# Optimization experiments

Hardware: AMD Instinct MI355X
Metric: run time of the kernel (lower is better)

## Reference

```python
import jax, jax.numpy as jnp
import numpy as np

N = 100000   # entities
T = 4        # edge types
E = 250000   # edges per type
D = 64       # dimension
H = 4        # attention heads
C = 64       # per-head out channels (PyG out_channels)
F_IN = 256   # raw feature dim
L = 2        # num_layers
NEG_SLOPE = 0.2


def setup_inputs() -> dict:
    key = jax.random.key(0)
    ks = jax.random.split(key, 10)
    return {
        "feature_matrix": jax.random.normal(ks[0], (N, F_IN), jnp.float32),
        "entity_emb": jax.random.normal(ks[1], (N + 1, D), jnp.float32),
        "lin_w": jax.random.normal(ks[2], (F_IN, D), jnp.float32) * 0.05,
        "lin_b": jnp.zeros((D,), jnp.float32),
        "ln_g": jnp.ones((D,), jnp.float32),
        "ln_b": jnp.zeros((D,), jnp.float32),
        "W_src": jax.random.normal(ks[3], (L, T, D, H * C), jnp.float32) * 0.1,
        "W_dst": jax.random.normal(ks[4], (L, T, D, H * C), jnp.float32) * 0.1,
        "a_src": jax.random.normal(ks[5], (L, T, H, C), jnp.float32) * 0.1,
        "a_dst": jax.random.normal(ks[6], (L, T, H, C), jnp.float32) * 0.1,
        "conv_bias": jnp.zeros((L, T, C), jnp.float32),
        "edge_index": jax.random.randint(ks[7], (T, 2, E), 0, N, jnp.int32),
    }


def _layer_norm(x, g, b):
    mu = jnp.mean(x, axis=-1, keepdims=True)
    var = jnp.var(x, axis=-1, keepdims=True)
    return (x - mu) * jax.lax.rsqrt(var + 1e-5) * g + b


def _l2_normalize(x):
    n = jnp.linalg.norm(x, axis=-1, keepdims=True)
    return x / jnp.maximum(n, 1e-12)


def _gat_conv(x, src, dst, Ws, Wd, a_s, a_d, bias):
    # x: [N, D]; src/dst: [E'] (self loops already appended, PyG default)
    xs = (x @ Ws).reshape(N, H, C)          # source projection per head
    xd = (x @ Wd).reshape(N, H, C)          # destination projection per head
    logit = (xs * a_s).sum(-1)[src] + (xd * a_d).sum(-1)[dst]  # [E', H]
    logit = jax.nn.leaky_relu(logit, NEG_SLOPE)
    # segment softmax over incoming edges of each dst node
    m = jax.lax.stop_gradient(jax.ops.segment_max(logit, dst, num_segments=N))
    p = jnp.exp(logit - m[dst])
    s = jax.ops.segment_sum(p, dst, num_segments=N)
    alpha = p / s[dst]                       # [E', H]
    msg = xs[src] * alpha[..., None]         # [E', H, C]
    out = jax.ops.segment_sum(msg.reshape(-1, H * C), dst, num_segments=N)
    out = out.reshape(N, H, C).mean(axis=1)  # concat=False -> head mean
    return out + bias


def reference(feature_matrix, entity_emb, lin_w, lin_b, ln_g, ln_b,
              W_src, W_dst, a_src, a_dst, conv_bias, edge_index):
    # feature_transform: Linear -> LayerNorm -> GELU (exact erf GELU, torch default)
    xf = jax.nn.gelu(_layer_norm(feature_matrix @ lin_w + lin_b, ln_g, ln_b),
                     approximate=False)
    xe = _l2_normalize(entity_emb[:N])
    x = xf + xe
    loop = jnp.arange(N, dtype=edge_index.dtype)
    for l in range(L):
        acc = jnp.zeros((N, C), x.dtype)
        for t in range(T):
            src = jnp.concatenate([edge_index[t, 0], loop])
            dst = jnp.concatenate([edge_index[t, 1], loop])
            acc = acc + _gat_conv(x, src, dst, W_src[l, t], W_dst[l, t],
                                  a_src[l, t], a_dst[l, t], conv_bias[l, t])
        x = jax.nn.gelu(acc / T, approximate=False)  # HeteroConv aggr='mean'; dropout=eval identity
    return x
```

## Files before the change

### kernel.cpp

```cpp
#include <hip/hip_runtime.h>
#include <hip/hip_bf16.h>
#include <cstdint>

#define NN   100000
#define TT   4
#define EE   250000
#define LL   2
#define NCH  49
#define N64  ((size_t)NN * 64)

typedef unsigned short ushort_t;
typedef __attribute__((ext_vector_type(8))) short bf16x8;
typedef __attribute__((ext_vector_type(16))) float floatx16;
typedef __attribute__((ext_vector_type(4))) float floatx4;

static __device__ __forceinline__ float gelu_exact(float v) {
    return 0.5f * v * (1.0f + erff(v * 0.7071067811865476f));
}
static __device__ __forceinline__ float wave_sum64(float v) {
    #pragma unroll
    for (int m = 32; m; m >>= 1) v += __shfl_xor(v, m, 64);
    return v;
}
static __device__ __forceinline__ ushort_t f2bf(float f) {
    unsigned u = __float_as_uint(f);
    u += 0x7FFFu + ((u >> 16) & 1u);
    return (ushort_t)(u >> 16);
}
static __device__ __forceinline__ float bf2f(ushort_t h) {
    return __uint_as_float((unsigned)h << 16);
}
static __device__ __forceinline__ void gl_lds16(const ushort_t* g, ushort_t* l) {
    __builtin_amdgcn_global_load_lds(
        (const __attribute__((address_space(1))) void*)g,
        (__attribute__((address_space(3))) void*)l, 16, 0, 0);
}

__global__ __launch_bounds__(256) void k_prep(
    const float* __restrict__ Wsrc, const float* __restrict__ Wdst,
    const float* __restrict__ asrc, const float* __restrict__ adst,
    const float* __restrict__ cb, const float* __restrict__ lin_w,
    ushort_t* __restrict__ wcTh, ushort_t* __restrict__ wcTl,
    ushort_t* __restrict__ lwTh, ushort_t* __restrict__ lwTl,
    ushort_t* __restrict__ bpTh, ushort_t* __restrict__ bpTl,
    float* __restrict__ bsum)
{
    int id = blockIdx.x * 256 + threadIdx.x;
    {
        int d = id & 63;
        int c = (id >> 6) & 63;
        int h = (id >> 12) & 3;
        int t = (id >> 14) & 3;
        int l = (id >> 16) & 1;
        float v = 0.25f * Wsrc[(((l * 4 + t) * 64 + d) * 256) + h * 64 + c];
        int dst = (l * 64 + c) * 1024 + (t * 256 + h * 64 + d);
        ushort_t hh = f2bf(v);
        bpTh[dst] = hh;
        bpTl[dst] = f2bf(v - bf2f(hh));
    }
    if (id < LL * 64 * 64) {
        int d   = id & 63;
        int col = (id >> 6) & 63;
        int l   = (id >> 12) & 1;
        int t = col >> 3, side = (col >> 2) & 1, h = col & 3;
        const float* W = side ? Wdst : Wsrc;
        const float* a = side ? adst : asrc;
        int wb = ((l * 4 + t) * 64 + d) * 256 + h * 64;
        int ab = ((l * 4 + t) * 4 + h) * 64;
        float s = 0.f;
        #pragma unroll 8
        for (int c2 = 0; c2 < 64; ++c2) s = fmaf(W[wb + c2], a[ab + c2], s);
        int dst = (l * 64 + col) * 64 + d;
        ushort_t hh = f2bf(s);
        wcTh[dst] = hh;
        wcTl[dst] = f2bf(s - bf2f(hh));
    }
    if (id < 64 * 256) {
        int k = id & 255, c = id >> 8;
        float v = lin_w[k * 64 + c];
        ushort_t hh = f2bf(v);
        lwTh[c * 256 + k] = hh;
        lwTl[c * 256 + k] = f2bf(v - bf2f(hh));
    }
    if (id < LL * 64) {
        int l = id >> 6, c = id & 63;
        float s = 0.f;
        for (int t = 0; t < TT; ++t) s += cb[(l * 4 + t) * 64 + c];
        bsum[id] = s;
    }
}

__global__ void k_hist(const int* __restrict__ ei, int* __restrict__ cursor) {
    int id = blockIdx.x * 256 + threadIdx.x;
    if (id >= TT * EE) return;
    int t = id / EE, e = id - t * EE;
    int d = ei[(t * 2 + 1) * EE + e];
    atomicAdd(&cursor[t * NN + d], 1);
}

__global__ __launch_bounds__(256) void k_scan1(const int* __restrict__ deg,
                                               int* __restrict__ csum) {
    int b = blockIdx.x, t = b / NCH, cc = b - t * NCH;
    int tid = threadIdx.x;
    int base = cc * 2048 + tid * 8;
    int s = 0;
    #pragma unroll
    for (int i = 0; i < 8; ++i) {
        int idx = base + i;
        if (idx < NN) s += deg[t * NN + idx];
    }
    #pragma unroll
    for (int m = 32; m; m >>= 1) s += __shfl_xor(s, m, 64);
    __shared__ int ws4[4];
    int lane = tid & 63, wid = tid >> 6;
    if (lane == 0) ws4[wid] = s;
    __syncthreads();
    if (tid == 0) csum[b] = ws4[0] + ws4[1] + ws4[2] + ws4[3];
}

__global__ void k_scan2(const int* __restrict__ csum, int* __restrict__ cbase,
                        int* __restrict__ row_ptr) {
    int t = threadIdx.x;
    if (t >= TT) return;
    int base = 0;
    for (int c = 0; c < NCH; ++c) {
        cbase[t * NCH + c] = base;
        base += csum[t * NCH + c];
    }
    row_ptr[t * (NN + 1) + NN] = base;
}

__global__ __launch_bounds__(256) void k_scan3(int* __restrict__ cursor,
                                               const int* __restrict__ cbase,
                                               int* __restrict__ row_ptr) {
    int b = blockIdx.x, t = b / NCH, cc = b - t * NCH;
    int tid = threadIdx.x, lane = tid & 63, wid = tid >> 6;
    int base = cc * 2048 + tid * 8;
    int vals[8], ts = 0;
    #pragma unroll
    for (int i = 0; i < 8; ++i) {
        int idx = base + i;
        int v = (idx < NN) ? cursor[t * NN + idx] : 0;
        vals[i] = v; ts += v;
    }
    int v = ts;
    #pragma unroll
    for (int off = 1; off < 64; off <<= 1) {
        int u = __shfl_up(v, off, 64);
        if (lane >= off) v += u;
    }
    __shared__ int wt[4];
    if (lane == 63) wt[wid] = v;
    __syncthreads();
    int wbase = 0;
    for (int w = 0; w < wid; ++w) wbase += wt[w];
    int run = cbase[t * NCH + cc] + wbase + (v - ts);
    #pragma unroll
    for (int i = 0; i < 8; ++i) {
        int idx = base + i;
        if (idx < NN) {
            row_ptr[t * (NN + 1) + idx] = run;
            cursor[t * NN + idx] = run;
        }
        run += vals[i];
    }
}

__global__ void k_scatter(const int* __restrict__ ei, int* __restrict__ cursor,
                          int2* __restrict__ sd) {
    int id = blockIdx.x * 256 + threadIdx.x;
    if (id >= TT * EE) return;
    int t = id / EE, r = id - t * EE;
    int s = ei[t * 2 * EE + r];
    int d = ei[(t * 2 + 1) * EE + r];
    int pos = atomicAdd(&cursor[t * NN + d], 1);
    sd[(size_t)t * EE + pos] = make_int2(s, d);
}

__global__ __launch_bounds__(256, 4) void k_gemm_f32a(
    const float* __restrict__ Af,
    const ushort_t* __restrict__ Bhi, const ushort_t* __restrict__ Blo,
    int K, int ldb, int nrows, float* __restrict__ Cout)
{
    constexpr int KC = 32;
    __shared__ ushort_t sAh[128 * 32], sAl[128 * 32];
    __shared__ ushort_t sBh[64 * 32],  sBl[64 * 32];
    const int tid = threadIdx.x;
    const int w = tid >> 6, ln = tid & 63;
    const int l31 = ln & 31, hl = ln >> 5;
    const int rowbase = blockIdx.x * 128;

    floatx16 accv[2];
    #pragma unroll
    for (int ct = 0; ct < 2; ++ct)
        #pragma unroll
        for (int r = 0; r < 16; ++r) accv[ct][r] = 0.f;

    for (int kc = 0; kc < K; kc += KC) {
        __syncthreads();
        #pragma unroll
        for (int i = 0; i < 2; ++i) {
            int f = tid + i * 256;
            int r = f >> 2, cg = f & 3;
            int row = rowbase + r;
            int sg = (r ^ (r >> 2)) & 3;
            int sw = r * 32 + ((cg ^ sg) << 3);
            if (row < nrows) {
                size_t ga = (size_t)row * K + kc + cg * 8;
                floatx4 v0 = *(const floatx4*)(Af + ga);
                floatx4 v1 = *(const floatx4*)(Af + ga + 4);
                float vf[8] = {v0.x, v0.y, v0.z, v0.w, v1.x, v1.y, v1.z, v1.w};
                unsigned hu[8], lu[8];
                #pragma unroll
                for (int q = 0; q < 8; ++q) {
                    ushort_t hh = f2bf(vf[q]);
                    hu[q] = hh;
                    lu[q] = f2bf(vf[q] - bf2f(hh));
                }
                uint4 H = make_uint4(hu[0] | (hu[1] << 16), hu[2] | (hu[3] << 16),
                                     hu[4] | (hu[5] << 16), hu[6] | (hu[7] << 16));
                uint4 L = make_uint4(lu[0] | (lu[1] << 16), lu[2] | (lu[3] << 16),
                                     lu[4] | (lu[5] << 16), lu[6] | (lu[7] << 16));
                *(uint4*)&sAh[sw] = H;
                *(uint4*)&sAl[sw] = L;
            } else {
                *(uint4*)&sAh[sw] = make_uint4(0, 0, 0, 0);
                *(uint4*)&sAl[sw] = make_uint4(0, 0, 0, 0);
            }
        }
        {
            int r = tid >> 2, cg = tid & 3;
            int sg = (r ^ (r >> 2)) & 3;
            int so = r * 32 + (cg << 3);
            size_t gb = (size_t)r * ldb + kc + ((cg ^ sg) << 3);
            gl_lds16(Bhi + gb, &sBh[so]);
            gl_lds16(Blo + gb, &sBl[so]);
        }
        __syncthreads();
        const int arow = (w << 5) + l31;
        const int sga = (arow ^ (arow >> 2)) & 3;
        const int sgb = (l31 ^ (l31 >> 2)) & 3;
        #pragma unroll
        for (int s = 0; s < 2; ++s) {
            const int c0 = (s << 1) | hl;
            const int ka = (c0 ^ sga) << 3;
            const int kb = (c0 ^ sgb) << 3;
            bf16x8 ah  = *(const bf16x8*)&sAh[arow * 32 + ka];
            bf16x8 al  = *(const bf16x8*)&sAl[arow * 32 + ka];
            bf16x8 bh0 = *(const bf16x8*)&sBh[l31 * 32 + kb];
            bf16x8 bl0 = *(const bf16x8*)&sBl[l31 * 32 + kb];
            bf16x8 bh1 = *(const bf16x8*)&sBh[(32 + l31) * 32 + kb];
            bf16x8 bl1 = *(const bf16x8*)&sBl[(32 + l31) * 32 + kb];
            accv[0] = __builtin_amdgcn_mfma_f32_32x32x16_bf16(ah, bh0, accv[0], 0, 0, 0);
            accv[1] = __builtin_amdgcn_mfma_f32_32x32x16_bf16(ah, bh1, accv[1], 0, 0, 0);
            accv[0] = __builtin_amdgcn_mfma_f32_32x32x16_bf16(al, bh0, accv[0], 0, 0, 0);
            accv[1] = __builtin_amdgcn_mfma_f32_32x32x16_bf16(al, bh1, accv[1], 0, 0, 0);
            accv[0] = __builtin_amdgcn_mfma_f32_32x32x16_bf16(ah, bl0, accv[0], 0, 0, 0);
            accv[1] = __builtin_amdgcn_mfma_f32_32x32x16_bf16(ah, bl1, accv[1], 0, 0, 0);
        }
    }
    #pragma unroll
    for (int ct = 0; ct < 2; ++ct) {
        int col = (ct << 5) + l31;
        #pragma unroll
        for (int r = 0; r < 16; ++r) {
            int row = rowbase + (w << 5) + (r & 3) + ((r >> 2) << 3) + (hl << 2);
            if (row < nrows) Cout[(size_t)row * 64 + col] = accv[ct][r];
        }
    }
}

template <int FLAGS>
__global__ __launch_bounds__(256, 6) void k_gemm64(
    const ushort_t* __restrict__ Ahi, const ushort_t* __restrict__ Alo,
    const ushort_t* __restrict__ Bhi, const ushort_t* __restrict__ Blo,
    int K, int ldb, int nrows,
    const float* __restrict__ accbuf, const float* __restrict__ bias,
    float* __restrict__ Cout)
{
    constexpr int KC = 32;
    __shared__ ushort_t sAh[64 * 32], sAl[64 * 32];
    __shared__ ushort_t sBh[64 * 32], sBl[64 * 32];
    const int tid = threadIdx.x;
    const int w = tid >> 6, ln = tid & 63;
    const int l31 = ln & 31, hl = ln >> 5;
    const int rt = w >> 1, ct = w & 1;
    const int rowbase = blockIdx.x * 64;

    floatx16 acc;
    #pragma unroll
    for (int r = 0; r < 16; ++r) acc[r] = 0.f;

    for (int kc = 0; kc < K; kc += KC) {
        __syncthreads();
        {
            int r = tid >> 2, cg = tid & 3;
            int sg = (r ^ (r >> 2)) & 3;
            int so = r * 32 + (cg << 3);
            int row = rowbase + r;
            if (row < nrows) {
                size_t ga = (size_t)row * K + kc + ((cg ^ sg) << 3);
                gl_lds16(Ahi + ga, &sAh[so]);
                gl_lds16(Alo + ga, &sAl[so]);
            }
            size_t gb = (size_t)r * ldb + kc + ((cg ^ sg) << 3);
            gl_lds16(Bhi + gb, &sBh[so]);
            gl_lds16(Blo + gb, &sBl[so]);
        }
        __syncthreads();
        const int arow = (rt << 5) + l31;
        const int brow = (ct << 5) + l31;
        const int sga = (arow ^ (arow >> 2)) & 3;
        const int sgb = (l31 ^ (l31 >> 2)) & 3;
        #pragma unroll
        for (int s = 0; s < 2; ++s) {
            const int c0 = (s << 1) | hl;
            const int ka = (c0 ^ sga) << 3;
            const int kb = (c0 ^ sgb) << 3;
            bf16x8 ah = *(const bf16x8*)&sAh[arow * 32 + ka];
            bf16x8 al = *(const bf16x8*)&sAl[arow * 32 + ka];
            bf16x8 bh = *(const bf16x8*)&sBh[brow * 32 + kb];
            bf16x8 bl = *(const bf16x8*)&sBl[brow * 32 + kb];
            acc = __builtin_amdgcn_mfma_f32_32x32x16_bf16(ah, bh, acc, 0, 0, 0);
            acc = __builtin_amdgcn_mfma_f32_32x32x16_bf16(al, bh, acc, 0, 0, 0);
            acc = __builtin_amdgcn_mfma_f32_32x32x16_bf16(ah, bl, acc, 0, 0, 0);
        }
    }
    int col = (ct << 5) + l31;
    float bv = (FLAGS & 2) ? bias[col] : 0.f;
    #pragma unroll
    for (int r = 0; r < 16; ++r) {
        int row = rowbase + (rt << 5) + (r & 3) + ((r >> 2) << 3) + (hl << 2);
        if (row < nrows) {
            size_t idx = (size_t)row * 64 + col;
            float v = acc[r];
            if (FLAGS & 1) v += accbuf[idx];
            if (FLAGS & 2) v = gelu_exact((v + bv) * 0.25f);
            Cout[idx] = v;
        }
    }
}

__global__ __launch_bounds__(256) void k_feat_post(
    const float* __restrict__ y, const float* __restrict__ lin_b,
    const float* __restrict__ ln_g, const float* __restrict__ ln_b,
    const float* __restrict__ emb, float* __restrict__ xout)
{
    int n = (blockIdx.x << 2) + (threadIdx.x >> 6);
    int c = threadIdx.x & 63;
    size_t base = (size_t)n * 64 + c;
    float v = y[base] + lin_b[c];
    float mean = wave_sum64(v) * 0.015625f;
    float t = v - mean;
    float var = wave_sum64(t * t) * 0.015625f;
    float vn = t * (1.0f / sqrtf(var + 1e-5f)) * ln_g[c] + ln_b[c];
    float g = gelu_exact(vn);
    float e = emb[base];
    float nrm = sqrtf(wave_sum64(e * e));
    float xv = g + e / fmaxf(nrm, 1e-12f);
    xout[base] = xv;
}

__global__ __launch_bounds__(256) void k_edgep(
    const float* __restrict__ s_all, const int2* __restrict__ sd,
    float* __restrict__ parr)
{
    int i = blockIdx.x * 256 + threadIdx.x;
    int t = blockIdx.y;
    if (i >= EE) return;
    size_t base = (size_t)t * EE + i;
    int2 e = sd[base];
    const float4 a = *(const float4*)&s_all[(size_t)e.x * 64 + t * 8];
    const float4 b = *(const float4*)&s_all[(size_t)e.y * 64 + t * 8 + 4];
    float l0 = a.x + b.x, l1 = a.y + b.y;
    float l2 = a.z + b.z, l3 = a.w + b.w;
    l0 = l0 > 0.f ? l0 : 0.2f * l0;
    l1 = l1 > 0.f ? l1 : 0.2f * l1;
    l2 = l2 > 0.f ? l2 : 0.2f * l2;
    l3 = l3 > 0.f ? l3 : 0.2f * l3;
    float4 p = make_float4(__expf(l0), __expf(l1), __expf(l2), __expf(l3));
    *(float4*)&parr[base * 4] = p;
}

__global__ __launch_bounds__(256) void k_edge2(
    const float* __restrict__ x, const float* __restrict__ s_all,
    const float* __restrict__ parr, const int* __restrict__ row_ptr,
    const int2* __restrict__ sd,
    ushort_t* __restrict__ zh, ushort_t* __restrict__ zl, int t0)
{
    int n = (blockIdx.x << 2) + (threadIdx.x >> 6);
    int lane = threadIdx.x & 63;
    const int tA = t0, tB = t0 + 1;
    int eA  = row_ptr[tA * (NN + 1) + n];
    int eA1 = row_ptr[tA * (NN + 1) + n + 1];
    int eB  = row_ptr[tB * (NN + 1) + n];
    int eB1 = row_ptr[tB * (NN + 1) + n + 1];
    const int*     sA = (const int*)(sd + (size_t)tA * EE);
    const floatx4* pA = (const floatx4*)parr + (size_t)tA * EE;
    const int*     sB = (const int*)(sd + (size_t)tB * EE);
    const floatx4* pB = (const floatx4*)parr + (size_t)tB * EE;
    float xn = x[(size_t)n * 64 + lane];
    float a0, a1, a2, a3, SA0, SA1, SA2, SA3;
    float b0, b1, b2, b3, SB0, SB1, SB2, SB3;
    {
        const float4 sa = *(const float4*)&s_all[(size_t)n * 64 + tA * 8];
        const float4 sb = *(const float4*)&s_all[(size_t)n * 64 + tA * 8 + 4];
        float l0 = sa.x + sb.x, l1 = sa.y + sb.y;
        float l2 = sa.z + sb.z, l3 = sa.w + sb.w;
        l0 = l0 > 0.f ? l0 : 0.2f * l0;  l1 = l1 > 0.f ? l1 : 0.2f * l1;
        l2 = l2 > 0.f ? l2 : 0.2f * l2;  l3 = l3 > 0.f ? l3 : 0.2f * l3;
        SA0 = __expf(l0); SA1 = __expf(l1); SA2 = __expf(l2); SA3 = __expf(l3);
        a0 = SA0 * xn; a1 = SA1 * xn; a2 = SA2 * xn; a3 = SA3 * xn;
    }
    {
        const float4 sa = *(const float4*)&s_all[(size_t)n * 64 + tB * 8];
        const float4 sb = *(const float4*)&s_all[(size_t)n * 64 + tB * 8 + 4];
        float l0 = sa.x + sb.x, l1 = sa.y + sb.y;
        float l2 = sa.z + sb.z, l3 = sa.w + sb.w;
        l0 = l0 > 0.f ? l0 : 0.2f * l0;  l1 = l1 > 0.f ? l1 : 0.2f * l1;
        l2 = l2 > 0.f ? l2 : 0.2f * l2;  l3 = l3 > 0.f ? l3 : 0.2f * l3;
        SB0 = __expf(l0); SB1 = __expf(l1); SB2 = __expf(l2); SB3 = __expf(l3);
        b0 = SB0 * xn; b1 = SB1 * xn; b2 = SB2 * xn; b3 = SB3 * xn;
    }
    int m = (eA1 - eA < eB1 - eB) ? (eA1 - eA) : (eB1 - eB);
    #pragma unroll 2
    for (int i = 0; i < m; ++i) {
        int sA_ = sA[2 * (eA + i)];
        int sB_ = sB[2 * (eB + i)];
        floatx4 pa = pA[eA + i];
        floatx4 pb = pB[eB + i];
        float xa = x[(size_t)sA_ * 64 + lane];
        float xb = x[(size_t)sB_ * 64 + lane];
        SA0 += pa.x; SA1 += pa.y; SA2 += pa.z; SA3 += pa.w;
        SB0 += pb.x; SB1 += pb.y; SB2 += pb.z; SB3 += pb.w;
        a0 = fmaf(pa.x, xa, a0); a1 = fmaf(pa.y, xa, a1);
        a2 = fmaf(pa.z, xa, a2); a3 = fmaf(pa.w, xa, a3);
        b0 = fmaf(pb.x, xb, b0); b1 = fmaf(pb.y, xb, b1);
        b2 = fmaf(pb.z, xb, b2); b3 = fmaf(pb.w, xb, b3);
    }
    eA += m; eB += m;
    for (; eA < eA1; ++eA) {
        int s = sA[2 * eA]; floatx4 p = pA[eA];
        float xv = x[(size_t)s * 64 + lane];
        SA0 += p.x; SA1 += p.y; SA2 += p.z; SA3 += p.w;
        a0 = fmaf(p.x, xv, a0); a1 = fmaf(p.y, xv, a1);
        a2 = fmaf(p.z, xv, a2); a3 = fmaf(p.w, xv, a3);
    }
    for (; eB < eB1; ++eB) {
        int s = sB[2 * eB]; floatx4 p = pB[eB];
        float xv = x[(size_t)s * 64 + lane];
        SB0 += p.x; SB1 += p.y; SB2 += p.z; SB3 += p.w;
        b0 = fmaf(p.x, xv, b0); b1 = fmaf(p.y, xv, b1);
        b2 = fmaf(p.z, xv, b2); b3 = fmaf(p.w, xv, b3);
    }
    size_t zb = (size_t)n * 512 + lane;
    {
        float v0 = a0 / SA0, v1 = a1 / SA1, v2 = a2 / SA2, v3 = a3 / SA3;
        ushort_t h0 = f2bf(v0), h1 = f2bf(v1), h2 = f2bf(v2), h3 = f2bf(v3);
        zh[zb]       = h0;  zl[zb]       = f2bf(v0 - bf2f(h0));
        zh[zb + 64]  = h1;  zl[zb + 64]  = f2bf(v1 - bf2f(h1));
        zh[zb + 128] = h2;  zl[zb + 128] = f2bf(v2 - bf2f(h2));
        zh[zb + 192] = h3;  zl[zb + 192] = f2bf(v3 - bf2f(h3));
    }
    {
        size_t zc = zb + 256;
        float v0 = b0 / SB0, v1 = b1 / SB1, v2 = b2 / SB2, v3 = b3 / SB3;
        ushort_t h0 = f2bf(v0), h1 = f2bf(v1), h2 = f2bf(v2), h3 = f2bf(v3);
        zh[zc]       = h0;  zl[zc]       = f2bf(v0 - bf2f(h0));
        zh[zc + 64]  = h1;  zl[zc + 64]  = f2bf(v1 - bf2f(h1));
        zh[zc + 128] = h2;  zl[zc + 128] = f2bf(v2 - bf2f(h2));
        zh[zc + 192] = h3;  zl[zc + 192] = f2bf(v3 - bf2f(h3));
    }
}

extern "C" void kernel_launch(void* const* d_in, const int* in_sizes, int n_in,
                              void* d_out, int out_size, void* d_ws, size_t ws_size,
                              hipStream_t stream) {
    const float* fm    = (const float*)d_in[0];
    const float* emb   = (const float*)d_in[1];
    const float* lin_w = (const float*)d_in[2];
    const float* lin_b = (const float*)d_in[3];
    const float* ln_g  = (const float*)d_in[4];
    const float* ln_b  = (const float*)d_in[5];
    const float* Wsrc  = (const float*)d_in[6];
    const float* Wdst  = (const float*)d_in[7];
    const float* asrc  = (const float*)d_in[8];
    const float* adst  = (const float*)d_in[9];
    const float* cbias = (const float*)d_in[10];
    const int*   ei    = (const int*)d_in[11];
    float* out = (float*)d_out;
    (void)in_sizes; (void)n_in; (void)out_size; (void)ws_size;

    char* w = (char*)d_ws;
    size_t off = 0;
    auto alloc = [&](size_t bytes) -> void* {
        void* p = w + off;
        off += (bytes + 255) & ~(size_t)255;
        return p;
    };
    ushort_t* wcTh = (ushort_t*)alloc((size_t)LL * 64 * 64 * 2);
    ushort_t* wcTl = (ushort_t*)alloc((size_t)LL * 64 * 64 * 2);
    ushort_t* lwTh = (ushort_t*)alloc((size_t)64 * 256 * 2);
    ushort_t* lwTl = (ushort_t*)alloc((size_t)64 * 256 * 2);
    ushort_t* bpTh = (ushort_t*)alloc((size_t)LL * 64 * 1024 * 2);
    ushort_t* bpTl = (ushort_t*)alloc((size_t)LL * 64 * 1024 * 2);
    float* bsum    = (float*)alloc((size_t)LL * 64 * 4);
    int*   row_ptr = (int*)  alloc((size_t)TT * (NN + 1) * 4);
    int*   cursor  = (int*)  alloc((size_t)TT * NN * 4);
    int2*  sdarr   = (int2*) alloc((size_t)TT * EE * 8);
    float* parr    = (float*)alloc((size_t)TT * EE * 4 * 4);
    int*   csum    = (int*)  alloc((size_t)TT * NCH * 4);
    int*   cbase   = (int*)  alloc((size_t)TT * NCH * 4);
    float* x       = (float*)alloc(N64 * 4);
    float* s_all   = (float*)alloc(N64 * 4);
    float* accB    = (float*)alloc(N64 * 4);
    size_t planeE = (size_t)NN * 512;
    ushort_t* zh = (ushort_t*)alloc(2 * planeE * 2);
    ushort_t* zl = zh + planeE;

    hipMemsetAsync(cursor, 0, (size_t)TT * NN * 4, stream);
    k_prep<<<512, 256, 0, stream>>>(Wsrc, Wdst, asrc, adst, cbias, lin_w,
                                    wcTh, wcTl, lwTh, lwTl, bpTh, bpTl, bsum);
    k_hist<<<(TT * EE + 255) / 256, 256, 0, stream>>>(ei, cursor);
    k_scan1<<<TT * NCH, 256, 0, stream>>>(cursor, csum);
    k_scan2<<<1, 64, 0, stream>>>(csum, cbase, row_ptr);
    k_scan3<<<TT * NCH, 256, 0, stream>>>(cursor, cbase, row_ptr);
    k_scatter<<<(TT * EE + 255) / 256, 256, 0, stream>>>(ei, cursor, sdarr);

    const int GB  = (NN + 127) / 128;
    const int GB2 = (NN + 63) / 64;
    k_gemm_f32a<<<GB, 256, 0, stream>>>(fm, lwTh, lwTl, 256, 256, NN, accB);
    k_feat_post<<<NN / 4, 256, 0, stream>>>(accB, lin_b, ln_g, ln_b, emb, x);

    const dim3 gp((EE + 255) / 256, TT);
    for (int l = 0; l < LL; ++l) {
        float* dest = (l == 0) ? x : out;
        k_gemm_f32a<<<GB, 256, 0, stream>>>(x, wcTh + l * 4096, wcTl + l * 4096,
                                            64, 64, NN, s_all);
        k_edgep<<<gp, 256, 0, stream>>>(s_all, sdarr, parr);
        const ushort_t* Bh = bpTh + (size_t)l * 65536;
        const ushort_t* Bl = bpTl + (size_t)l * 65536;
        k_edge2<<<NN / 4, 256, 0, stream>>>(x, s_all, parr, row_ptr, sdarr,
                                            zh, zl, 0);
        k_gemm64<0><<<GB2, 256, 0, stream>>>(zh, zl, Bh, Bl, 512, 1024, NN,
                                             nullptr, nullptr, accB);
        k_edge2<<<NN / 4, 256, 0, stream>>>(x, s_all, parr, row_ptr, sdarr,
                                            zh, zl, 2);
        k_gemm64<3><<<GB2, 256, 0, stream>>>(zh, zl, Bh + 512, Bl + 512, 512, 1024,
                                             NN, accB, bsum + l * 64, dest);
    }
}
```

Baseline: 1.019 ms.

## Store edge aggregates as fp32 and split to bf16 hi/lo inside GEMM

The edge aggregation kernel now writes fp32 results instead of two bf16 hi/lo planes. The GEMM loads fp32 A tiles and does the hi/lo split itself before writing to LDS, replacing the async global-to-LDS copies. Each edge wave now handles two nodes (n and n+N/2) so more independent gather loads are in flight. The intermediate traffic stays the same size (fp32 equals hi+lo bf16), but the GEMM adds conversion ALU work and loses the direct LDS loads, while the edge kernel uses more registers.

```diff
diff --git a/kernel.cpp b/kernel.cpp
--- a/kernel.cpp
+++ b/kernel.cpp
@@ -271,8 +271,8 @@
 }
 
 template <int FLAGS>
-__global__ __launch_bounds__(256, 6) void k_gemm64(
-    const ushort_t* __restrict__ Ahi, const ushort_t* __restrict__ Alo,
+__global__ __launch_bounds__(256, 6) void k_gemm64f(
+    const float* __restrict__ Af,
     const ushort_t* __restrict__ Bhi, const ushort_t* __restrict__ Blo,
     int K, int ldb, int nrows,
     const float* __restrict__ accbuf, const float* __restrict__ bias,
@@ -296,13 +296,31 @@
         {
             int r = tid >> 2, cg = tid & 3;
             int sg = (r ^ (r >> 2)) & 3;
+            int row = rowbase + r;
+            int sw = r * 32 + ((cg ^ sg) << 3);
+            if (row < nrows) {
+                size_t ga = (size_t)row * K + kc + cg * 8;
+                floatx4 v0 = *(const floatx4*)(Af + ga);
+                floatx4 v1 = *(const floatx4*)(Af + ga + 4);
+                float vf[8] = {v0.x, v0.y, v0.z, v0.w, v1.x, v1.y, v1.z, v1.w};
+                unsigned hu[8], lu[8];
+                #pragma unroll
+                for (int q = 0; q < 8; ++q) {
+                    ushort_t hh = f2bf(vf[q]);
+                    hu[q] = hh;
+                    lu[q] = f2bf(vf[q] - bf2f(hh));
+                }
+                uint4 H = make_uint4(hu[0] | (hu[1] << 16), hu[2] | (hu[3] << 16),
+                                     hu[4] | (hu[5] << 16), hu[6] | (hu[7] << 16));
+                uint4 L = make_uint4(lu[0] | (lu[1] << 16), lu[2] | (lu[3] << 16),
+                                     lu[4] | (lu[5] << 16), lu[6] | (lu[7] << 16));
+                *(uint4*)&sAh[sw] = H;
+                *(uint4*)&sAl[sw] = L;
+            } else {
+                *(uint4*)&sAh[sw] = make_uint4(0, 0, 0, 0);
+                *(uint4*)&sAl[sw] = make_uint4(0, 0, 0, 0);
+            }
             int so = r * 32 + (cg << 3);
-            int row = rowbase + r;
-            if (row < nrows) {
-                size_t ga = (size_t)row * K + kc + ((cg ^ sg) << 3);
-                gl_lds16(Ahi + ga, &sAh[so]);
-                gl_lds16(Alo + ga, &sAl[so]);
-            }
             size_t gb = (size_t)r * ldb + kc + ((cg ^ sg) << 3);
             gl_lds16(Bhi + gb, &sBh[so]);
             gl_lds16(Blo + gb, &sBl[so]);
@@ -382,94 +400,181 @@
     *(float4*)&parr[base * 4] = p;
 }
 
-__global__ __launch_bounds__(256) void k_edge2(
+__global__ __launch_bounds__(256, 6) void k_edge2(
     const float* __restrict__ x, const float* __restrict__ s_all,
     const float* __restrict__ parr, const int* __restrict__ row_ptr,
-    const int2* __restrict__ sd,
-    ushort_t* __restrict__ zh, ushort_t* __restrict__ zl, int t0)
+    const int2* __restrict__ sd, float* __restrict__ zf, int t0)
 {
-    int n = (blockIdx.x << 2) + (threadIdx.x >> 6);
+    int id = (blockIdx.x << 2) + (threadIdx.x >> 6);
     int lane = threadIdx.x & 63;
+    const int nA = id, nC = id + (NN / 2);
     const int tA = t0, tB = t0 + 1;
-    int eA  = row_ptr[tA * (NN + 1) + n];
-    int eA1 = row_ptr[tA * (NN + 1) + n + 1];
-    int eB  = row_ptr[tB * (NN + 1) + n];
-    int eB1 = row_ptr[tB * (NN + 1) + n + 1];
-    const int*     sA = (const int*)(sd + (size_t)tA * EE);
-    const floatx4* pA = (const floatx4*)parr + (size_t)tA * EE;
-    const int*     sB = (const int*)(sd + (size_t)tB * EE);
-    const floatx4* pB = (const floatx4*)parr + (size_t)tB * EE;
-    float xn = x[(size_t)n * 64 + lane];
+    int eA = row_ptr[tA * (NN + 1) + nA], eA1 = row_ptr[tA * (NN + 1) + nA + 1];
+    int eB = row_ptr[tB * (NN + 1) + nA], eB1 = row_ptr[tB * (NN + 1) + nA + 1];
+    int eC = row_ptr[tA * (NN + 1) + nC], eC1 = row_ptr[tA * (NN + 1) + nC + 1];
+    int eD = row_ptr[tB * (NN + 1) + nC], eD1 = row_ptr[tB * (NN + 1) + nC + 1];
+    const int*     sAp = (const int*)(sd + (size_t)tA * EE);
+    const floatx4* pAp = (const floatx4*)parr + (size_t)tA * EE;
+    const int*     sBp = (const int*)(sd + (size_t)tB * EE);
+    const floatx4* pBp = (const floatx4*)parr + (size_t)tB * EE;
+
+    float xnA = x[(size_t)nA * 64 + lane];
+    float xnC = x[(size_t)nC * 64 + lane];
+
     float a0, a1, a2, a3, SA0, SA1, SA2, SA3;
     float b0, b1, b2, b3, SB0, SB1, SB2, SB3;
-    {
-        const float4 sa = *(const float4*)&s_all[(size_t)n * 64 + tA * 8];
-        const float4 sb = *(const float4*)&s_all[(size_t)n * 64 + tA * 8 + 4];
+    float c0, c1, c2, c3, SC0, SC1, SC2, SC3;
+    float d0, d1, d2, d3, SD0, SD1, SD2, SD3;
+    {
+        const float4 sa = *(const float4*)&s_all[(size_t)nA * 64 + tA * 8];
+        const float4 sb = *(const float4*)&s_all[(size_t)nA * 64 + tA * 8 + 4];
         float l0 = sa.x + sb.x, l1 = sa.y + sb.y;
         float l2 = sa.z + sb.z, l3 = sa.w + sb.w;
         l0 = l0 > 0.f ? l0 : 0.2f * l0;  l1 = l1 > 0.f ? l1 : 0.2f * l1;
         l2 = l2 > 0.f ? l2 : 0.2f * l2;  l3 = l3 > 0.f ? l3 : 0.2f * l3;
         SA0 = __expf(l0); SA1 = __expf(l1); SA2 = __expf(l2); SA3 = __expf(l3);
-        a0 = SA0 * xn; a1 = SA1 * xn; a2 = SA2 * xn; a3 = SA3 * xn;
-    }
-    {
-        const float4 sa = *(const float4*)&s_all[(size_t)n * 64 + tB * 8];
-        const float4 sb = *(const float4*)&s_all[(size_t)n * 64 + tB * 8 + 4];
+        a0 = SA0 * xnA; a1 = SA1 * xnA; a2 = SA2 * xnA; a3 = SA3 * xnA;
+    }
+    {
+        const float4 sa = *(const float4*)&s_all[(size_t)nA * 64 + tB * 8];
+        const float4 sb = *(const float4*)&s_all[(size_t)nA * 64 + tB * 8 + 4];
         float l0 = sa.x + sb.x, l1 = sa.y + sb.y;
         float l2 = sa.z + sb.z, l3 = sa.w + sb.w;
         l0 = l0 > 0.f ? l0 : 0.2f * l0;  l1 = l1 > 0.f ? l1 : 0.2f * l1;
         l2 = l2 > 0.f ? l2 : 0.2f * l2;  l3 = l3 > 0.f ? l3 : 0.2f * l3;
         SB0 = __expf(l0); SB1 = __expf(l1); SB2 = __expf(l2); SB3 = __expf(l3);
-        b0 = SB0 * xn; b1 = SB1 * xn; b2 = SB2 * xn; b3 = SB3 * xn;
-    }
-    int m = (eA1 - eA < eB1 - eB) ? (eA1 - eA) : (eB1 - eB);
-    #pragma unroll 2
-    for (int i = 0; i < m; ++i) {
-        int sA_ = sA[2 * (eA + i)];
-        int sB_ = sB[2 * (eB + i)];
-        floatx4 pa = pA[eA + i];
-        floatx4 pb = pB[eB + i];
-        float xa = x[(size_t)sA_ * 64 + lane];
-        float xb = x[(size_t)sB_ * 64 + lane];
+        b0 = SB0 * xnA; b1 = SB1 * xnA; b2 = SB2 * xnA; b3 = SB3 * xnA;
+    }
+    {
+        const float4 sa = *(const float4*)&s_all[(size_t)nC * 64 + tA * 8];
+        const float4 sb = *(const float4*)&s_all[(size_t)nC * 64 + tA * 8 + 4];
+        float l0 = sa.x + sb.x, l1 = sa.y + sb.y;
+        float l2 = sa.z + sb.z, l3 = sa.w + sb.w;
+        l0 = l0 > 0.f ? l0 : 0.2f * l0;  l1 = l1 > 0.f ? l1 : 0.2f * l1;
+        l2 = l2 > 0.f ? l2 : 0.2f * l2;  l3 = l3 > 0.f ? l3 : 0.2f * l3;
+        SC0 = __expf(l0); SC1 = __expf(l1); SC2 = __expf(l2); SC3 = __expf(l3);
+        c0 = SC0 * xnC; c1 = SC1 * xnC; c2 = SC2 * xnC; c3 = SC3 * xnC;
+    }
+    {
+        const float4 sa = *(const float4*)&s_all[(size_t)nC * 64 + tB * 8];
+        const float4 sb = *(const float4*)&s_all[(size_t)nC * 64 + tB * 8 + 4];
+        float l0 = sa.x + sb.x, l1 = sa.y + sb.y;
+        float l2 = sa.z + sb.z, l3 = sa.w + sb.w;
+        l0 = l0 > 0.f ? l0 : 0.2f * l0;  l1 = l1 > 0.f ? l1 : 0.2f * l1;
+        l2 = l2 > 0.f ? l2 : 0.2f * l2;  l3 = l3 > 0.f ? l3 : 0.2f * l3;
+        SD0 = __expf(l0); SD1 = __expf(l1); SD2 = __expf(l2); SD3 = __expf(l3);
+        d0 = SD0 * xnC; d1 = SD1 * xnC; d2 = SD2 * xnC; d3 = SD3 * xnC;
+    }
+    int m4a = (eA1 - eA < eB1 - eB) ? (eA1 - eA) : (eB1 - eB);
+    int m4b = (eC1 - eC < eD1 - eD) ? (eC1 - eC) : (eD1 - eD);
+    int m4 = (m4a < m4b) ? m4a : m4b;
+    #pragma unroll 1
+    for (int q = 0; q < m4; ++q) {
+        int sA = sAp[2 * (eA + q)];
+        int sB = sBp[2 * (eB + q)];
+        int sC = sAp[2 * (eC + q)];
+        int sD = sBp[2 * (eD + q)];
+        floatx4 pa = pAp[eA + q];
+        floatx4 pb = pBp[eB + q];
+        floatx4 pc = pAp[eC + q];
+        floatx4 pd = pBp[eD + q];
+        float xa = x[(size_t)sA * 64 + lane];
+        float xb = x[(size_t)sB * 64 + lane];
+        float xc = x[(size_t)sC * 64 + lane];
+        float xd = x[(size_t)sD * 64 + lane];
         SA0 += pa.x; SA1 += pa.y; SA2 += pa.z; SA3 += pa.w;
         SB0 += pb.x; SB1 += pb.y; SB2 += pb.z; SB3 += pb.w;
+        SC0 += pc.x; SC1 += pc.y; SC2 += pc.z; SC3 += pc.w;
+        SD0 += pd.x; SD1 += pd.y; SD2 += pd.z; SD3 += pd.w;
         a0 = fmaf(pa.x, xa, a0); a1 = fmaf(pa.y, xa, a1);
         a2 = fmaf(pa.z, xa, a2); a3 = fmaf(pa.w, xa, a3);
         b0 = fmaf(pb.x, xb, b0); b1 = fmaf(pb.y, xb, b1);
         b2 = fmaf(pb.z, xb, b2); b3 = fmaf(pb.w, xb, b3);
-    }
-    eA += m; eB += m;
+        c0 = fmaf(pc.x, xc, c0); c1 = fmaf(pc.y, xc, c1);
+        c2 = fmaf(pc.z, xc, c2); c3 = fmaf(pc.w, xc, c3);
+        d0 = fmaf(pd.x, xd, d0); d1 = fmaf(pd.y, xd, d1);
+        d2 = fmaf(pd.z, xd, d2); d3 = fmaf(pd.w, xd, d3);
+    }
+    eA += m4; eB += m4; eC += m4; eD += m4;
+    {
+        int m2 = (eA1 - eA < eB1 - eB) ? (eA1 - eA) : (eB1 - eB);
+        #pragma unroll 2
+        for (int q = 0; q < m2; ++q) {
+            int sA = sAp[2 * (eA + q)];
+            int sB = sBp[2 * (eB + q)];
+            floatx4 pa = pAp[eA + q];
+            floatx4 pb = pBp[eB + q];
+            float xa = x[(size_t)sA * 64 + lane];
+            float xb = x[(size_t)sB * 64 + lane];
+            SA0 += pa.x; SA1 += pa.y; SA2 += pa.z; SA3 += pa.w;
+            SB0 += pb.x; SB1 += pb.y; SB2 += pb.z; SB3 += pb.w;
+            a0 = fmaf(pa.x, xa, a0); a1 = fmaf(pa.y, xa, a1);
+            a2 = fmaf(pa.z, xa, a2); a3 = fmaf(pa.w, xa, a3);
+            b0 = fmaf(pb.x, xb, b0); b1 = fmaf(pb.y, xb, b1);
+            b2 = fmaf(pb.z, xb, b2); b3 = fmaf(pb.w, xb, b3);
+        }
+        eA += m2; eB += m2;
+    }
+    {
+        int m2 = (eC1 - eC < eD1 - eD) ? (eC1 - eC) : (eD1 - eD);
+        #pragma unroll 2
+        for (int q = 0; q < m2; ++q) {
+            int sC = sAp[2 * (eC + q)];
+            int sD = sBp[2 * (eD + q)];
+            floatx4 pc = pAp[eC + q];
+            floatx4 pd = pBp[eD + q];
+            float xc = x[(size_t)sC * 64 + lane];
+            float xd = x[(size_t)sD * 64 + lane];
+            SC0 += pc.x; SC1 += pc.y; SC2 += pc.z; SC3 += pc.w;
+            SD0 += pd.x; SD1 += pd.y; SD2 += pd.z; SD3 += pd.w;
+            c0 = fmaf(pc.x, xc, c0); c1 = fmaf(pc.y, xc, c1);
+            c2 = fmaf(pc.z, xc, c2); c3 = fmaf(pc.w, xc, c3);
+            d0 = fmaf(pd.x, xd, d0); d1 = fmaf(pd.y, xd, d1);
+            d2 = fmaf(pd.z, xd, d2); d3 = fmaf(pd.w, xd, d3);
+        }
+        eC += m2; eD += m2;
+    }
     for (; eA < eA1; ++eA) {
-        int s = sA[2 * eA]; floatx4 p = pA[eA];
+        int s = sAp[2 * eA]; floatx4 p = pAp[eA];
         float xv = x[(size_t)s * 64 + lane];
         SA0 += p.x; SA1 += p.y; SA2 += p.z; SA3 += p.w;
         a0 = fmaf(p.x, xv, a0); a1 = fmaf(p.y, xv, a1);
         a2 = fmaf(p.z, xv, a2); a3 = fmaf(p.w, xv, a3);
     }
     for (; eB < eB1; ++eB) {
-        int s = sB[2 * eB]; floatx4 p = pB[eB];
+        int s = sBp[2 * eB]; floatx4 p = pBp[eB];
         float xv = x[(size_t)s * 64 + lane];
         SB0 += p.x; SB1 += p.y; SB2 += p.z; SB3 += p.w;
         b0 = fmaf(p.x, xv, b0); b1 = fmaf(p.y, xv, b1);
         b2 = fmaf(p.z, xv, b2); b3 = fmaf(p.w, xv, b3);
     }
-    size_t zb = (size_t)n * 512 + lane;
-    {
-        float v0 = a0 / SA0, v1 = a1 / SA1, v2 = a2 / SA2, v3 = a3 / SA3;
-        ushort_t h0 = f2bf(v0), h1 = f2bf(v1), h2 = f2bf(v2), h3 = f2bf(v3);
-        zh[zb]       = h0;  zl[zb]       = f2bf(v0 - bf2f(h0));
-        zh[zb + 64]  = h1;  zl[zb + 64]  = f2bf(v1 - bf2f(h1));
-        zh[zb + 128] = h2;  zl[zb + 128] = f2bf(v2 - bf2f(h2));
-        zh[zb + 192] = h3;  zl[zb + 192] = f2bf(v3 - bf2f(h3));
-    }
-    {
-        size_t zc = zb + 256;
-        float v0 = b0 / SB0, v1 = b1 / SB1, v2 = b2 / SB2, v3 = b3 / SB3;
-        ushort_t h0 = f2bf(v0), h1 = f2bf(v1), h2 = f2bf(v2), h3 = f2bf(v3);
-        zh[zc]       = h0;  zl[zc]       = f2bf(v0 - bf2f(h0));
-        zh[zc + 64]  = h1;  zl[zc + 64]  = f2bf(v1 - bf2f(h1));
-        zh[zc + 128] = h2;  zl[zc + 128] = f2bf(v2 - bf2f(h2));
-        zh[zc + 192] = h3;  zl[zc + 192] = f2bf(v3 - bf2f(h3));
+    for (; eC < eC1; ++eC) {
+        int s = sAp[2 * eC]; floatx4 p = pAp[eC];
+        float xv = x[(size_t)s * 64 + lane];
+        SC0 += p.x; SC1 += p.y; SC2 += p.z; SC3 += p.w;
+        c0 = fmaf(p.x, xv, c0); c1 = fmaf(p.y, xv, c1);
+        c2 = fmaf(p.z, xv, c2); c3 = fmaf(p.w, xv, c3);
+    }
+    for (; eD < eD1; ++eD) {
+        int s = sBp[2 * eD]; floatx4 p = pBp[eD];
+        float xv = x[(size_t)s * 64 + lane];
+        SD0 += p.x; SD1 += p.y; SD2 += p.z; SD3 += p.w;
+        d0 = fmaf(p.x, xv, d0); d1 = fmaf(p.y, xv, d1);
+        d2 = fmaf(p.z, xv, d2); d3 = fmaf(p.w, xv, d3);
+    }
+    {
+        size_t zb = (size_t)nA * 512 + lane;
+        zf[zb]       = a0 / SA0;  zf[zb + 64]  = a1 / SA1;
+        zf[zb + 128] = a2 / SA2;  zf[zb + 192] = a3 / SA3;
+        zf[zb + 256] = b0 / SB0;  zf[zb + 320] = b1 / SB1;
+        zf[zb + 384] = b2 / SB2;  zf[zb + 448] = b3 / SB3;
+    }
+    {
+        size_t zb = (size_t)nC * 512 + lane;
+        zf[zb]       = c0 / SC0;  zf[zb + 64]  = c1 / SC1;
+        zf[zb + 128] = c2 / SC2;  zf[zb + 192] = c3 / SC3;
+        zf[zb + 256] = d0 / SD0;  zf[zb + 320] = d1 / SD1;
+        zf[zb + 384] = d2 / SD2;  zf[zb + 448] = d3 / SD3;
     }
 }
 
@@ -514,9 +619,7 @@
     float* x       = (float*)alloc(N64 * 4);
     float* s_all   = (float*)alloc(N64 * 4);
     float* accB    = (float*)alloc(N64 * 4);
-    size_t planeE = (size_t)NN * 512;
-    ushort_t* zh = (ushort_t*)alloc(2 * planeE * 2);
-    ushort_t* zl = zh + planeE;
+    float* zf = (float*)alloc((size_t)NN * 512 * 4);
 
     hipMemsetAsync(cursor, 0, (size_t)TT * NN * 4, stream);
     k_prep<<<512, 256, 0, stream>>>(Wsrc, Wdst, asrc, adst, cbias, lin_w,
@@ -540,13 +643,11 @@
         k_edgep<<<gp, 256, 0, stream>>>(s_all, sdarr, parr);
         const ushort_t* Bh = bpTh + (size_t)l * 65536;
         const ushort_t* Bl = bpTl + (size_t)l * 65536;
-        k_edge2<<<NN / 4, 256, 0, stream>>>(x, s_all, parr, row_ptr, sdarr,
-                                            zh, zl, 0);
-        k_gemm64<0><<<GB2, 256, 0, stream>>>(zh, zl, Bh, Bl, 512, 1024, NN,
-                                             nullptr, nullptr, accB);
-        k_edge2<<<NN / 4, 256, 0, stream>>>(x, s_all, parr, row_ptr, sdarr,
-                                            zh, zl, 2);
-        k_gemm64<3><<<GB2, 256, 0, stream>>>(zh, zl, Bh + 512, Bl + 512, 512, 1024,
-                                             NN, accB, bsum + l * 64, dest);
-    }
-}
+        k_edge2<<<NN / 8, 256, 0, stream>>>(x, s_all, parr, row_ptr, sdarr, zf, 0);
+        k_gemm64f<0><<<GB2, 256, 0, stream>>>(zf, Bh, Bl, 512, 1024, NN,
+                                              nullptr, nullptr, accB);
+        k_edge2<<<NN / 8, 256, 0, stream>>>(x, s_all, parr, row_ptr, sdarr, zf, 2);
+        k_gemm64f<3><<<GB2, 256, 0, stream>>>(zf, Bh + 512, Bl + 512, 512, 1024,
+                                              NN, accB, bsum + l * 64, dest);
+    }
+}
```

After: 1.021 ms. No clear change (+0.2%).

## Process one edge type per pass with fp32 intermediate split inside GEMM

Applied to the files above, without the earlier changes.

The edge aggregation now handles a single edge type per launch, with each wave covering two destination nodes half the graph apart. It writes fp32 aggregated features instead of precomputed bf16 hi/lo planes. The GEMM loads the fp32 A tile and does the hi/lo bf16 split while staging it into shared memory. The aim is to shrink the intermediate buffer and cut memory traffic, at the cost of twice as many launches and extra conversion work in the GEMM, plus accumulation through accB across four passes.

```diff
diff --git a/kernel.cpp b/kernel.cpp
--- a/kernel.cpp
+++ b/kernel.cpp
@@ -271,8 +271,8 @@
 }
 
 template <int FLAGS>
-__global__ __launch_bounds__(256, 6) void k_gemm64(
-    const ushort_t* __restrict__ Ahi, const ushort_t* __restrict__ Alo,
+__global__ __launch_bounds__(256, 6) void k_gemm64f(
+    const float* __restrict__ Af,
     const ushort_t* __restrict__ Bhi, const ushort_t* __restrict__ Blo,
     int K, int ldb, int nrows,
     const float* __restrict__ accbuf, const float* __restrict__ bias,
@@ -296,13 +296,31 @@
         {
             int r = tid >> 2, cg = tid & 3;
             int sg = (r ^ (r >> 2)) & 3;
+            int row = rowbase + r;
+            int sw = r * 32 + ((cg ^ sg) << 3);
+            if (row < nrows) {
+                size_t ga = (size_t)row * K + kc + cg * 8;
+                floatx4 v0 = *(const floatx4*)(Af + ga);
+                floatx4 v1 = *(const floatx4*)(Af + ga + 4);
+                float vf[8] = {v0.x, v0.y, v0.z, v0.w, v1.x, v1.y, v1.z, v1.w};
+                unsigned hu[8], lu[8];
+                #pragma unroll
+                for (int q = 0; q < 8; ++q) {
+                    ushort_t hh = f2bf(vf[q]);
+                    hu[q] = hh;
+                    lu[q] = f2bf(vf[q] - bf2f(hh));
+                }
+                uint4 H = make_uint4(hu[0] | (hu[1] << 16), hu[2] | (hu[3] << 16),
+                                     hu[4] | (hu[5] << 16), hu[6] | (hu[7] << 16));
+                uint4 L = make_uint4(lu[0] | (lu[1] << 16), lu[2] | (lu[3] << 16),
+                                     lu[4] | (lu[5] << 16), lu[6] | (lu[7] << 16));
+                *(uint4*)&sAh[sw] = H;
+                *(uint4*)&sAl[sw] = L;
+            } else {
+                *(uint4*)&sAh[sw] = make_uint4(0, 0, 0, 0);
+                *(uint4*)&sAl[sw] = make_uint4(0, 0, 0, 0);
+            }
             int so = r * 32 + (cg << 3);
-            int row = rowbase + r;
-            if (row < nrows) {
-                size_t ga = (size_t)row * K + kc + ((cg ^ sg) << 3);
-                gl_lds16(Ahi + ga, &sAh[so]);
-                gl_lds16(Alo + ga, &sAl[so]);
-            }
             size_t gb = (size_t)r * ldb + kc + ((cg ^ sg) << 3);
             gl_lds16(Bhi + gb, &sBh[so]);
             gl_lds16(Blo + gb, &sBl[so]);
@@ -385,91 +403,81 @@
 __global__ __launch_bounds__(256) void k_edge2(
     const float* __restrict__ x, const float* __restrict__ s_all,
     const float* __restrict__ parr, const int* __restrict__ row_ptr,
-    const int2* __restrict__ sd,
-    ushort_t* __restrict__ zh, ushort_t* __restrict__ zl, int t0)
+    const int2* __restrict__ sd, float* __restrict__ zf, int t)
 {
-    int n = (blockIdx.x << 2) + (threadIdx.x >> 6);
+    int id = (blockIdx.x << 2) + (threadIdx.x >> 6);
     int lane = threadIdx.x & 63;
-    const int tA = t0, tB = t0 + 1;
-    int eA  = row_ptr[tA * (NN + 1) + n];
-    int eA1 = row_ptr[tA * (NN + 1) + n + 1];
-    int eB  = row_ptr[tB * (NN + 1) + n];
-    int eB1 = row_ptr[tB * (NN + 1) + n + 1];
-    const int*     sA = (const int*)(sd + (size_t)tA * EE);
-    const floatx4* pA = (const floatx4*)parr + (size_t)tA * EE;
-    const int*     sB = (const int*)(sd + (size_t)tB * EE);
-    const floatx4* pB = (const floatx4*)parr + (size_t)tB * EE;
-    float xn = x[(size_t)n * 64 + lane];
+    const int nA = id, nC = id + (NN / 2);
+    int eA = row_ptr[t * (NN + 1) + nA], eA1 = row_ptr[t * (NN + 1) + nA + 1];
+    int eC = row_ptr[t * (NN + 1) + nC], eC1 = row_ptr[t * (NN + 1) + nC + 1];
+    const int*     sp = (const int*)(sd + (size_t)t * EE);
+    const floatx4* pp = (const floatx4*)parr + (size_t)t * EE;
+
+    float xnA = x[(size_t)nA * 64 + lane];
+    float xnC = x[(size_t)nC * 64 + lane];
+
     float a0, a1, a2, a3, SA0, SA1, SA2, SA3;
-    float b0, b1, b2, b3, SB0, SB1, SB2, SB3;
+    float c0, c1, c2, c3, SC0, SC1, SC2, SC3;
     {
-        const float4 sa = *(const float4*)&s_all[(size_t)n * 64 + tA * 8];
-        const float4 sb = *(const float4*)&s_all[(size_t)n * 64 + tA * 8 + 4];
+        const float4 sa = *(const float4*)&s_all[(size_t)nA * 64 + t * 8];
+        const float4 sb = *(const float4*)&s_all[(size_t)nA * 64 + t * 8 + 4];
         float l0 = sa.x + sb.x, l1 = sa.y + sb.y;
         float l2 = sa.z + sb.z, l3 = sa.w + sb.w;
         l0 = l0 > 0.f ? l0 : 0.2f * l0;  l1 = l1 > 0.f ? l1 : 0.2f * l1;
         l2 = l2 > 0.f ? l2 : 0.2f * l2;  l3 = l3 > 0.f ? l3 : 0.2f * l3;
         SA0 = __expf(l0); SA1 = __expf(l1); SA2 = __expf(l2); SA3 = __expf(l3);
-        a0 = SA0 * xn; a1 = SA1 * xn; a2 = SA2 * xn; a3 = SA3 * xn;
+        a0 = SA0 * xnA; a1 = SA1 * xnA; a2 = SA2 * xnA; a3 = SA3 * xnA;
     }
     {
-        const float4 sa = *(const float4*)&s_all[(size_t)n * 64 + tB * 8];
-        const float4 sb = *(const float4*)&s_all[(size_t)n * 64 + tB * 8 + 4];
+        const float4 sa = *(const float4*)&s_all[(size_t)nC * 64 + t * 8];
+        const float4 sb = *(const float4*)&s_all[(size_t)nC * 64 + t * 8 + 4];
         float l0 = sa.x + sb.x, l1 = sa.y + sb.y;
         float l2 = sa.z + sb.z, l3 = sa.w + sb.w;
         l0 = l0 > 0.f ? l0 : 0.2f * l0;  l1 = l1 > 0.f ? l1 : 0.2f * l1;
         l2 = l2 > 0.f ? l2 : 0.2f * l2;  l3 = l3 > 0.f ? l3 : 0.2f * l3;
-        SB0 = __expf(l0); SB1 = __expf(l1); SB2 = __expf(l2); SB3 = __expf(l3);
-        b0 = SB0 * xn; b1 = SB1 * xn; b2 = SB2 * xn; b3 = SB3 * xn;
-    }
-    int m = (eA1 - eA < eB1 - eB) ? (eA1 - eA) : (eB1 - eB);
+        SC0 = __expf(l0); SC1 = __expf(l1); SC2 = __expf(l2); SC3 = __expf(l3);
+        c0 = SC0 * xnC; c1 = SC1 * xnC; c2 = SC2 * xnC; c3 = SC3 * xnC;
+    }
+    int m = (eA1 - eA < eC1 - eC) ? (eA1 - eA) : (eC1 - eC);
     #pragma unroll 2
-    for (int i = 0; i < m; ++i) {
-        int sA_ = sA[2 * (eA + i)];
-        int sB_ = sB[2 * (eB + i)];
-        floatx4 pa = pA[eA + i];
-        floatx4 pb = pB[eB + i];
-        float xa = x[(size_t)sA_ * 64 + lane];
-        float xb = x[(size_t)sB_ * 64 + lane];
+    for (int q = 0; q < m; ++q) {
+        int sA = sp[2 * (eA + q)];
+        int sC = sp[2 * (eC + q)];
+        floatx4 pa = pp[eA + q];
+        floatx4 pc = pp[eC + q];
+        float xa = x[(size_t)sA * 64 + lane];
+        float xc = x[(size_t)sC * 64 + lane];
         SA0 += pa.x; SA1 += pa.y; SA2 += pa.z; SA3 += pa.w;
-        SB0 += pb.x; SB1 += pb.y; SB2 += pb.z; SB3 += pb.w;
+        SC0 += pc.x; SC1 += pc.y; SC2 += pc.z; SC3 += pc.w;
         a0 = fmaf(pa.x, xa, a0); a1 = fmaf(pa.y, xa, a1);
         a2 = fmaf(pa.z, xa, a2); a3 = fmaf(pa.w, xa, a3);
-        b0 = fmaf(pb.x, xb, b0); b1 = fmaf(pb.y, xb, b1);
-        b2 = fmaf(pb.z, xb, b2); b3 = fmaf(pb.w, xb, b3);
-    }
-    eA += m; eB += m;
+        c0 = fmaf(pc.x, xc, c0); c1 = fmaf(pc.y, xc, c1);
+        c2 = fmaf(pc.z, xc, c2); c3 = fmaf(pc.w, xc, c3);
+    }
+    eA += m; eC += m;
     for (; eA < eA1; ++eA) {
-        int s = sA[2 * eA]; floatx4 p = pA[eA];
+        int s = sp[2 * eA]; floatx4 p = pp[eA];
         float xv = x[(size_t)s * 64 + lane];
         SA0 += p.x; SA1 += p.y; SA2 += p.z; SA3 += p.w;
         a0 = fmaf(p.x, xv, a0); a1 = fmaf(p.y, xv, a1);
         a2 = fmaf(p.z, xv, a2); a3 = fmaf(p.w, xv, a3);
     }
-    for (; eB < eB1; ++eB) {
-        int s = sB[2 * eB]; floatx4 p = pB[eB];
+    for (; eC < eC1; ++eC) {
+        int s = sp[2 * eC]; floatx4 p = pp[eC];
         float xv = x[(size_t)s * 64 + lane];
-        SB0 += p.x; SB1 += p.y; SB2 += p.z; SB3 += p.w;
-        b0 = fmaf(p.x, xv, b0); b1 = fmaf(p.y, xv, b1);
-        b2 = fmaf(p.z, xv, b2); b3 = fmaf(p.w, xv, b3);
-    }
-    size_t zb = (size_t)n * 512 + lane;
+        SC0 += p.x; SC1 += p.y; SC2 += p.z; SC3 += p.w;
+        c0 = fmaf(p.x, xv, c0); c1 = fmaf(p.y, xv, c1);
+        c2 = fmaf(p.z, xv, c2); c3 = fmaf(p.w, xv, c3);
+    }
     {
-        float v0 = a0 / SA0, v1 = a1 / SA1, v2 = a2 / SA2, v3 = a3 / SA3;
-        ushort_t h0 = f2bf(v0), h1 = f2bf(v1), h2 = f2bf(v2), h3 = f2bf(v3);
-        zh[zb]       = h0;  zl[zb]       = f2bf(v0 - bf2f(h0));
-        zh[zb + 64]  = h1;  zl[zb + 64]  = f2bf(v1 - bf2f(h1));
-        zh[zb + 128] = h2;  zl[zb + 128] = f2bf(v2 - bf2f(h2));
-        zh[zb + 192] = h3;  zl[zb + 192] = f2bf(v3 - bf2f(h3));
+        size_t zb = (size_t)nA * 256 + lane;
+        zf[zb]       = a0 / SA0;  zf[zb + 64]  = a1 / SA1;
+        zf[zb + 128] = a2 / SA2;  zf[zb + 192] = a3 / SA3;
     }
     {
-        size_t zc = zb + 256;
-        float v0 = b0 / SB0, v1 = b1 / SB1, v2 = b2 / SB2, v3 = b3 / SB3;
-        ushort_t h0 = f2bf(v0), h1 = f2bf(v1), h2 = f2bf(v2), h3 = f2bf(v3);
-        zh[zc]       = h0;  zl[zc]       = f2bf(v0 - bf2f(h0));
-        zh[zc + 64]  = h1;  zl[zc + 64]  = f2bf(v1 - bf2f(h1));
-        zh[zc + 128] = h2;  zl[zc + 128] = f2bf(v2 - bf2f(h2));
-        zh[zc + 192] = h3;  zl[zc + 192] = f2bf(v3 - bf2f(h3));
+        size_t zb = (size_t)nC * 256 + lane;
+        zf[zb]       = c0 / SC0;  zf[zb + 64]  = c1 / SC1;
+        zf[zb + 128] = c2 / SC2;  zf[zb + 192] = c3 / SC3;
     }
 }
 
@@ -514,9 +522,7 @@
     float* x       = (float*)alloc(N64 * 4);
     float* s_all   = (float*)alloc(N64 * 4);
     float* accB    = (float*)alloc(N64 * 4);
-    size_t planeE = (size_t)NN * 512;
-    ushort_t* zh = (ushort_t*)alloc(2 * planeE * 2);
-    ushort_t* zl = zh + planeE;
+    float* zf = (float*)alloc((size_t)NN * 256 * 4);
 
     hipMemsetAsync(cursor, 0, (size_t)TT * NN * 4, stream);
     k_prep<<<512, 256, 0, stream>>>(Wsrc, Wdst, asrc, adst, cbias, lin_w,
@@ -540,13 +546,21 @@
         k_edgep<<<gp, 256, 0, stream>>>(s_all, sdarr, parr);
         const ushort_t* Bh = bpTh + (size_t)l * 65536;
         const ushort_t* Bl = bpTl + (size_t)l * 65536;
-        k_edge2<<<NN / 4, 256, 0, stream>>>(x, s_all, parr, row_ptr, sdarr,
-                                            zh, zl, 0);
-        k_gemm64<0><<<GB2, 256, 0, stream>>>(zh, zl, Bh, Bl, 512, 1024, NN,
-                                             nullptr, nullptr, accB);
-        k_edge2<<<NN / 4, 256, 0, stream>>>(x, s_all, parr, row_ptr, sdarr,
-                                            zh, zl, 2);
-        k_gemm64<3><<<GB2, 256, 0, stream>>>(zh, zl, Bh + 512, Bl + 512, 512, 1024,
-                                             NN, accB, bsum + l * 64, dest);
-    }
-}
+        for (int t = 0; t < TT; ++t) {
+            k_edge2<<<NN / 8, 256, 0, stream>>>(x, s_all, parr, row_ptr,
+                                                sdarr, zf, t);
+            if (t == 0)
+                k_gemm64f<0><<<GB2, 256, 0, stream>>>(zf, Bh + t * 256, Bl + t * 256,
+                                                      256, 1024, NN,
+                                                      nullptr, nullptr, accB);
+            else if (t < TT - 1)
+                k_gemm64f<1><<<GB2, 256, 0, stream>>>(zf, Bh + t * 256, Bl + t * 256,
+                                                      256, 1024, NN,
+                                                      accB, nullptr, accB);
+            else
+                k_gemm64f<3><<<GB2, 256, 0, stream>>>(zf, Bh + t * 256, Bl + t * 256,
+                                                      256, 1024, NN,
+                                                      accB, bsum + l * 64, dest);
+        }
+    }
+}
```

New measurement: 969.3 us. -4.9%, faster.
